# Kernel tuning notes

Hardware: AMD Instinct MI355X
Metric: run time of the kernel (lower is better)

Reference implementation:

```python
import jax, jax.numpy as jnp
import numpy as np

QMIN, QMAX = -128.0, 127.0

@jax.custom_vjp
def ste_round(x):
    return jnp.round(x)

def _ste_fwd(x):
    return jnp.round(x), None

def _ste_bwd(_, g):
    return (g,)

ste_round.defvjp(_ste_fwd, _ste_bwd)

def fake_quant_act(x, scale):
    # Int8 per-tensor fake quant: q = clip(round(x/s)) * s
    return jnp.clip(ste_round(x / scale), QMIN, QMAX) * scale

def fake_quant_weight(w):
    # Int8WeightPerTensorFloat: scale from max-abs statistic
    s = jnp.max(jnp.abs(w)) / QMAX
    return jnp.clip(ste_round(w / s), QMIN, QMAX) * s

def conv2d(x, w, b, pad):
    y = jax.lax.conv_general_dilated(
        x, w, window_strides=(1, 1), padding=[(pad, pad), (pad, pad)],
        dimension_numbers=('NCHW', 'OIHW', 'NCHW'))
    return y + b[None, :, None, None]

def maxpool2(x):
    return jax.lax.reduce_window(
        x, -jnp.inf, jax.lax.max, (1, 1, 2, 2), (1, 1, 2, 2), 'VALID')

def setup_inputs() -> dict:
    key = jax.random.key(0)
    ks = jax.random.split(key, 12)
    def w_init(k, shape, fan_in):
        return jax.random.normal(k, shape, jnp.float32) * (1.0 / np.sqrt(fan_in))
    inp = {
        'x': jax.random.normal(ks[0], (32, 1, 256, 256), jnp.float32),
        'w1': w_init(ks[1], (16, 1, 3, 3), 1 * 9),
        'b1': jax.random.normal(ks[2], (16,), jnp.float32) * 0.01,
        'w2': w_init(ks[3], (32, 16, 3, 3), 16 * 9),
        'b2': jax.random.normal(ks[4], (32,), jnp.float32) * 0.01,
        'w3': w_init(ks[5], (32, 32, 5, 5), 32 * 25),
        'b3': jax.random.normal(ks[6], (32,), jnp.float32) * 0.01,
        'w4': w_init(ks[7], (16, 32, 3, 3), 32 * 9),
        'b4': jax.random.normal(ks[8], (16,), jnp.float32) * 0.01,
        'wc': w_init(ks[9], (10, 16), 16),
        'bc': jax.random.normal(ks[10], (10,), jnp.float32) * 0.01,
        # 11 learned per-tensor activation scales, kept strictly positive
        'act_scales': jax.random.uniform(ks[11], (11,), jnp.float32) * 0.05 + 0.01,
    }
    return inp

def reference(x, w1, b1, w2, b2, w3, b3, w4, b4, wc, bc, act_scales):
    s = act_scales
    x = fake_quant_act(x, s[0])                                  # input_quant
    x = conv2d(x, fake_quant_weight(w1), b1, 0)                  # conv1 (3x3, p0)
    x = fake_quant_act(jax.nn.relu(x), s[1])                     # relu1
    x = fake_quant_act(x, s[2])                                  # quant1
    x = conv2d(x, fake_quant_weight(w2), b2, 1)                  # conv2 (3x3, p1)
    x = fake_quant_act(jax.nn.relu(x), s[3])                     # relu2
    x = fake_quant_act(x, s[4])                                  # quant2
    x = conv2d(x, fake_quant_weight(w3), b3, 2)                  # conv3 (5x5, p2)
    x = fake_quant_act(jax.nn.relu(x), s[5])                     # relu3
    x = fake_quant_act(x, s[6])                                  # quant3
    x = maxpool2(x)                                              # pool1
    x = fake_quant_act(x, s[7])                                  # pool1_quant
    x = conv2d(x, fake_quant_weight(w4), b4, 0)                  # conv4 (3x3, p0)
    x = fake_quant_act(jax.nn.relu(x), s[8])                     # relu4
    x = fake_quant_act(x, s[9])                                  # quant4
    x = jnp.mean(x, axis=(2, 3))                                 # global avg pool -> [B,16]
    x = fake_quant_act(x, s[10])                                 # pool_quant
    return x @ fake_quant_weight(wc).T + bc                      # classifier -> [B,10]
```

## Files before the change

kernel.cpp:

```cpp
#include <hip/hip_runtime.h>
#include <math.h>


typedef int i32x4  __attribute__((ext_vector_type(4)));
typedef int i32x16 __attribute__((ext_vector_type(16)));

__device__ __forceinline__ int quant_clip(float v) {
  float r = rintf(v);
  r = fminf(fmaxf(r, -128.0f), 127.0f);
  return (int)r;
}

__device__ __forceinline__ int pack4i8(int q0, int q1, int q2, int q3) {
  return (q0 & 255) | ((q1 & 255) << 8) | ((q2 & 255) << 16) | ((q3 & 255) << 24);
}

__global__ __launch_bounds__(256) void k_quant_weights(
    const float* __restrict__ w1, const float* __restrict__ w2,
    const float* __restrict__ w3, const float* __restrict__ w4,
    const float* __restrict__ wc, float* __restrict__ wscale,
    int* __restrict__ qw1, int* __restrict__ qw2B, int* __restrict__ qw3B,
    int* __restrict__ qw4B, int* __restrict__ qwc)
{
  __shared__ float red[256];
  __shared__ float ssh;
  const int t = blockIdx.x, tid = threadIdx.x;
  const float* src = (t == 0) ? w1 : (t == 1) ? w2 : (t == 2) ? w3 : (t == 3) ? w4 : wc;
  const int nsrc   = (t == 0) ? 144 : (t == 1) ? 4608 : (t == 2) ? 25600 : (t == 3) ? 4608 : 160;

  float m = 0.0f;
  for (int i = tid; i < nsrc; i += 256) m = fmaxf(m, fabsf(src[i]));
  red[tid] = m;
  __syncthreads();
  for (int s = 128; s > 0; s >>= 1) {
    if (tid < s) red[tid] = fmaxf(red[tid], red[tid + s]);
    __syncthreads();
  }
  if (tid == 0) { ssh = red[0] / 127.0f; wscale[t] = ssh; }
  __syncthreads();
  const float s = ssh;

  if (t == 0) {
    for (int i = tid; i < 144; i += 256) qw1[i] = quant_clip(w1[i] / s);
  } else if (t == 1) {
    for (int wi = tid; wi < 1536; wi += 256) {
      int step = wi >> 8, rem = wi & 255;
      int ln = rem >> 2, w = rem & 3;
      int oc = ln & 31, h = ln >> 5;
      int ky = step >> 1, kxp = (step & 1) * 2;
      int q[4];
      #pragma unroll
      for (int j = 0; j < 4; j++) {
        int k = h * 16 + w * 4 + j;
        int ic = k & 15, kx = kxp + (k >> 4);
        float val = (kx < 3) ? w2[((oc * 16 + ic) * 3 + ky) * 3 + kx] : 0.0f;
        q[j] = quant_clip(val / s);
      }
      qw2B[wi] = pack4i8(q[0], q[1], q[2], q[3]);
    }
  } else if (t == 2) {
    for (int wi = tid; wi < 6400; wi += 256) {
      int tap = wi >> 8, rem = wi & 255;
      int ln = rem >> 2, w = rem & 3;
      int oc = ln & 31, h = ln >> 5;
      int ky = tap / 5, kx = tap % 5;
      int q[4];
      #pragma unroll
      for (int j = 0; j < 4; j++) {
        int ic = h * 16 + w * 4 + j;
        q[j] = quant_clip(w3[((oc * 32 + ic) * 5 + ky) * 5 + kx] / s);
      }
      qw3B[wi] = pack4i8(q[0], q[1], q[2], q[3]);
    }
  } else if (t == 3) {
    for (int wi = tid; wi < 1280; wi += 256) {
      int mf = wi >> 8, rem = wi & 255;
      int ln = rem >> 2, w = rem & 3;
      int oc = ln & 15, chunk = ln >> 4;
      int tp = 2 * mf + (chunk >> 1);
      int half = chunk & 1;
      int q[4];
      #pragma unroll
      for (int j = 0; j < 4; j++) {
        float val = 0.0f;
        if (tp < 9) {
          int ky = tp / 3, kx = tp % 3;
          int ic = half * 16 + w * 4 + j;
          val = w4[((oc * 32 + ic) * 3 + ky) * 3 + kx];
        }
        q[j] = quant_clip(val / s);
      }
      qw4B[wi] = pack4i8(q[0], q[1], q[2], q[3]);
    }
  } else {
    for (int wi = tid; wi < 40; wi += 256) {
      int o = wi / 4, i4 = wi % 4;
      int q[4];
      #pragma unroll
      for (int j = 0; j < 4; j++) q[j] = quant_clip(wc[o * 16 + i4 * 4 + j] / s);
      qwc[wi] = pack4i8(q[0], q[1], q[2], q[3]);
    }
  }
}

__global__ __launch_bounds__(256) void k_quant_input(
    const float* __restrict__ x, const float* __restrict__ scales,
    int* __restrict__ q0w)
{
  int i = blockIdx.x * 256 + threadIdx.x;
  if (i >= 524288) return;
  float inv = 1.0f / scales[0];
  float4 v = ((const float4*)x)[i];
  q0w[i] = pack4i8(quant_clip(v.x * inv), quant_clip(v.y * inv),
                   quant_clip(v.z * inv), quant_clip(v.w * inv));
}

__global__ __launch_bounds__(256) void k_zero_border(int* __restrict__ a2p)
{
  int i = blockIdx.x * 256 + threadIdx.x;
  int n = i >> 11, p = i & 2047;
  int row, col;
  if (p < 1032) {
    int rb = p / 258;
    row = (rb < 2) ? rb : 254 + rb;
    col = p % 258;
  } else {
    int q = p - 1032;
    int cb = q & 3;
    col = (cb < 2) ? cb : 254 + cb;
    row = 2 + (q >> 2);
  }
  int4* dst = (int4*)(a2p + (((size_t)n * 258 + row) * 258 + col) * 8);
  dst[0] = make_int4(0, 0, 0, 0);
  dst[1] = make_int4(0, 0, 0, 0);
}

__global__ __launch_bounds__(256) void k_conv1(
    const signed char* __restrict__ q0, const int* __restrict__ qw1,
    const float* __restrict__ b1, const float* __restrict__ scales,
    const float* __restrict__ wscale, int* __restrict__ a1)
{
  __shared__ int wsh[144];
  __shared__ signed char lut[128];
  if (threadIdx.x < 144) wsh[threadIdx.x] = qw1[threadIdx.x];
  if (threadIdx.x < 128) {
    float s1 = scales[1], inv2 = 1.0f / scales[2];
    lut[threadIdx.x] =
        (signed char)(int)fminf(rintf(((float)threadIdx.x * s1) * inv2), 127.0f);
  }
  __syncthreads();

  int pix = blockIdx.x * 256 + threadIdx.x;
  const int TOT = 32 * 254 * 254;
  if (pix >= TOT) return;
  int n = pix / (254 * 254), r = pix % (254 * 254);
  int oy = r / 254, ox = r % 254;

  int av[9];
  const signed char* base = q0 + (n * 256 + oy) * 256 + ox;
  #pragma unroll
  for (int ky = 0; ky < 3; ky++)
    #pragma unroll
    for (int kx = 0; kx < 3; kx++)
      av[ky * 3 + kx] = (int)base[ky * 256 + kx];

  float inv1 = 1.0f / scales[1];
  float scl = scales[0] * wscale[0];
  int outw[4];
  #pragma unroll
  for (int g = 0; g < 4; g++) {
    int q[4];
    #pragma unroll
    for (int j = 0; j < 4; j++) {
      int oc = g * 4 + j;
      int acc = 0;
      #pragma unroll
      for (int k = 0; k < 9; k++) acc += av[k] * wsh[oc * 9 + k];
      float y = fmaf(scl, (float)acc, b1[oc]);
      int idx = (int)fminf(fmaxf(rintf(y * inv1), 0.0f), 127.0f);
      q[j] = lut[idx];
    }
    outw[g] = pack4i8(q[0], q[1], q[2], q[3]);
  }
  *(int4*)(a1 + pix * 4) = make_int4(outw[0], outw[1], outw[2], outw[3]);
}

__global__ __launch_bounds__(256) void k_conv2_mfma(
    const int* __restrict__ a1, const int* __restrict__ qw2B,
    const float* __restrict__ b2, const float* __restrict__ scales,
    const float* __restrict__ wscale, signed char* __restrict__ a2p)
{
  __shared__ signed char lut[128];
  if (threadIdx.x < 128) {
    float s3 = scales[3], inv4 = 1.0f / scales[4];
    lut[threadIdx.x] =
        (signed char)(int)fminf(rintf(((float)threadIdx.x * s3) * inv4), 127.0f);
  }
  __syncthreads();

  const int lane = threadIdx.x & 63;
  const int bid = blockIdx.x;
  const int swz = (bid & 7) * 256 + (bid >> 3);
  const int gw = swz * 4 + (threadIdx.x >> 6);

  i32x4 bw[6];
  #pragma unroll
  for (int t = 0; t < 6; t++)
    bw[t] = *(const i32x4*)(qw2B + (t * 64 + lane) * 4);

  const float inv3 = 1.0f / scales[3];
  const float scl = scales[2] * wscale[1];
  const int oc = lane & 31, h = lane >> 5, rr = lane & 31;
  const float bias = b2[oc];

  const int TILES = 32 * 254 * 8;
  #pragma unroll 1
  for (int t8 = 0; t8 < 8; t8++) {
    int tile = gw * 8 + t8;
    if (tile >= TILES) break;
    int n = tile / (254 * 8);
    int r = tile % (254 * 8);
    int y = r >> 3, X0 = (r & 7) * 32;

    i32x4 Af[6];
    #pragma unroll
    for (int ky = 0; ky < 3; ky++) {
      int iy = y + ky - 1;
      bool vy = (iy >= 0) && (iy < 254);
      int iyc = min(max(iy, 0), 253);
      #pragma unroll
      for (int kp = 0; kp < 2; kp++) {
        int ix = X0 + rr + kp * 2 + h - 1;
        bool vx = (ix >= 0) && (ix < 254);
        int ixc = min(max(ix, 0), 253);
        i32x4 a = *(const i32x4*)(a1 + ((n * 254 + iyc) * 254 + ixc) * 4);
        bool v = vy && vx;
        i32x4 z;
        z[0] = v ? a[0] : 0; z[1] = v ? a[1] : 0;
        z[2] = v ? a[2] : 0; z[3] = v ? a[3] : 0;
        Af[ky * 2 + kp] = z;
      }
    }

    i32x16 acc0, acc1;
    #pragma unroll
    for (int z = 0; z < 16; z++) { acc0[z] = 0; acc1[z] = 0; }
    #pragma unroll
    for (int ky = 0; ky < 3; ky++) {
      acc0 = __builtin_amdgcn_mfma_i32_32x32x32_i8(Af[ky * 2 + 0], bw[ky * 2 + 0], acc0, 0, 0, 0);
      acc1 = __builtin_amdgcn_mfma_i32_32x32x32_i8(Af[ky * 2 + 1], bw[ky * 2 + 1], acc1, 0, 0, 0);
    }

    #pragma unroll
    for (int q = 0; q < 4; q++) {
      #pragma unroll
      for (int j = 0; j < 4; j++) {
        int row = j + 8 * q + 4 * h;
        int x = X0 + row;
        int accv = acc0[q * 4 + j] + acc1[q * 4 + j];
        float yv = fmaf(scl, (float)accv, bias);
        int idx = (int)fminf(fmaxf(rintf(yv * inv3), 0.0f), 127.0f);
        if (x < 254)
          a2p[((size_t)(n * 258 + (y + 2)) * 258 + (x + 2)) * 32 + oc] =
              lut[idx];
      }
    }
  }
}

__global__ __launch_bounds__(256, 3) void k_conv3pool_mfma(
    const signed char* __restrict__ a2p, const int* __restrict__ qw3B,
    const float* __restrict__ b3, const float* __restrict__ scales,
    const float* __restrict__ wscale, signed char* __restrict__ a3p)
{
  __shared__ __align__(16) signed char ash[8 * 2176];
  __shared__ int bsh[6400];
  __shared__ signed char lut56[128];
  __shared__ signed char lut67[128];

  const int tid = threadIdx.x;
  const int lane = tid & 63;
  const int w = tid >> 6;

  const int bid = blockIdx.x;
  const int swz = (bid & 7) * 256 + (bid >> 3);
  const int n  = swz >> 6;
  const int Xg = (swz >> 4) & 3;
  const int Yq = swz & 15;
  const int c0 = 64 * Xg;

  const int oc = lane & 31, h = lane >> 5;
  const int rr = lane & 31;
  const int pp = rr >> 2, dy = (rr >> 1) & 1, dx = rr & 1;
  const int xl = 8 * w + pp;
  const int colb = (2 * xl + dx) * 32 + h * 16;
  const int X0w = 32 * Xg + 8 * w;

  const float inv5 = 1.0f / scales[5];
  const float scl = scales[4] * wscale[2];
  const float bias = b3[oc];

  {
    const int4* srcB = (const int4*)qw3B;
    int4* dstB = (int4*)bsh;
    for (int i = tid; i < 1600; i += 256) dstB[i] = srcB[i];
    if (tid < 128) {
      float s5 = scales[5], s6 = scales[6];
      float inv6 = 1.0f / s6, inv7 = 1.0f / scales[7];
      lut56[tid] = (signed char)(int)fminf(rintf(((float)tid * s5) * inv6), 127.0f);
      lut67[tid] = (signed char)(int)fminf(rintf(((float)tid * s6) * inv7), 127.0f);
    }
  }

  #pragma unroll 1
  for (int it = 0; it < 4; ++it) {
    const int Yp = 4 * Yq + it;
    const int r0 = 4 * Yp;

    __syncthreads();
    for (int ci = tid; ci < 1088; ci += 256) {
      int row = ci / 136;
      int cr = ci - row * 136;
      int col = cr >> 1, half = cr & 1;
      int gr = min(r0 + row, 257);
      int gc = min(c0 + col, 257);
      const int4* srcA = (const int4*)(a2p +
          (((size_t)n * 258 + gr) * 258 + gc) * 32 + half * 16);
      *(int4*)(&ash[row * 2176 + cr * 16]) = *srcA;
    }
    __syncthreads();

    i32x16 acc0, acc1;
    #pragma unroll
    for (int z = 0; z < 16; z++) { acc0[z] = 0; acc1[z] = 0; }

    i32x4 F0[5], F1[5], F2[5], F3[5];

#define LOAD_ROW(F, J)                                                   \
    {                                                                    \
      const signed char* rbase = &ash[(dy + (J)) * 2176 + colb];         \
      _Pragma("unroll")                                                  \
      for (int kx = 0; kx < 5; kx++)                                     \
        F[kx] = *(const i32x4*)(rbase + kx * 32);                        \
    }
#define STEP(KY, RA, RB)                                                 \
    {                                                                    \
      _Pragma("unroll")                                                  \
      for (int kx = 0; kx < 5; kx++) {                                   \
        i32x4 bfrag = *(const i32x4*)&bsh[(((KY) * 5 + kx) * 64 + lane) * 4]; \
        acc0 = __builtin_amdgcn_mfma_i32_32x32x32_i8(RA[kx], bfrag, acc0, 0, 0, 0); \
        acc1 = __builtin_amdgcn_mfma_i32_32x32x32_i8(RB[kx], bfrag, acc1, 0, 0, 0); \
      }                                                                  \
    }

    LOAD_ROW(F0, 0) LOAD_ROW(F1, 1) LOAD_ROW(F2, 2)
    LOAD_ROW(F3, 3) STEP(0, F0, F2)
    LOAD_ROW(F0, 4) STEP(1, F1, F3)
    LOAD_ROW(F1, 5) STEP(2, F2, F0)
    LOAD_ROW(F2, 6) STEP(3, F3, F1)
    STEP(4, F0, F2)
#undef LOAD_ROW
#undef STEP

    #pragma unroll
    for (int ty = 0; ty < 2; ty++) {
      int Y = 2 * Yp + ty;
      #pragma unroll
      for (int q = 0; q < 4; q++) {
        int b = 2 * q + h;
        int X = X0w + b;
        int a0, a1v, a2, a3;
        if (ty == 0) {
          a0 = acc0[q * 4 + 0]; a1v = acc0[q * 4 + 1];
          a2 = acc0[q * 4 + 2]; a3 = acc0[q * 4 + 3];
        } else {
          a0 = acc1[q * 4 + 0]; a1v = acc1[q * 4 + 1];
          a2 = acc1[q * 4 + 2]; a3 = acc1[q * 4 + 3];
        }
        int am = max(max(a0, a1v), max(a2, a3));
        float yv = fmaf(scl, (float)am, bias);
        int r1 = (int)fminf(fmaxf(rintf(yv * inv5), 0.0f), 127.0f);
        int r2 = lut56[r1];
        int r3 = lut67[r2];
        if (X < 127 && Y < 127)
          a3p[((size_t)(n * 127 + Y) * 127 + X) * 32 + oc] = (signed char)r3;
      }
    }
  }
}

__global__ __launch_bounds__(256) void k_conv4_mfma(
    const signed char* __restrict__ a3p, const int* __restrict__ qw4B,
    const float* __restrict__ b4, const float* __restrict__ scales,
    const float* __restrict__ wscale, signed char* __restrict__ a4b)
{
  __shared__ signed char lut[128];
  if (threadIdx.x < 128) {
    float s8 = scales[8], inv9 = 1.0f / scales[9];
    lut[threadIdx.x] =
        (signed char)(int)fminf(rintf(((float)threadIdx.x * s8) * inv9), 127.0f);
  }
  __syncthreads();

  const int lane = threadIdx.x & 63;
  const int bid = blockIdx.x;
  const int swz = (bid & 7) * 256 + (bid >> 3);
  const int gw = swz * 4 + (threadIdx.x >> 6);

  i32x4 bw[5];
  #pragma unroll
  for (int t = 0; t < 5; t++)
    bw[t] = *(const i32x4*)(qw4B + (t * 64 + lane) * 4);

  const int chunk = lane >> 4;
  int offB[5];
  #pragma unroll
  for (int mf = 0; mf < 5; mf++) {
    int tp = 2 * mf + (chunk >> 1);
    if (tp > 8) tp = 8;
    int ky = tp / 3, kx = tp % 3;
    offB[mf] = (ky * 127 + kx) * 32 + (chunk & 1) * 16;
  }

  const float inv8 = 1.0f / scales[8];
  const float scl = scales[7] * wscale[3];
  const int oc = lane & 15;
  const float bias = b4[oc];
  const int arow = lane & 15;

  const int TILES = 32 * 125 * 8;
  #pragma unroll 1
  for (int t4 = 0; t4 < 4; t4++) {
    int tile = gw * 4 + t4;
    if (tile >= TILES) break;
    int n = tile / 1000;
    int r = tile % 1000;
    int y = r >> 3, X0 = (r & 7) * 16;

    const signed char* base =
        a3p + ((size_t)n * 16129 + (size_t)y * 127 + (X0 + arow)) * 32;

    i32x4 Af[5];
    #pragma unroll
    for (int mf = 0; mf < 5; mf++)
      Af[mf] = *(const i32x4*)(base + offB[mf]);

    i32x4 acc;
    acc[0] = 0; acc[1] = 0; acc[2] = 0; acc[3] = 0;
    #pragma unroll
    for (int mf = 0; mf < 5; mf++)
      acc = __builtin_amdgcn_mfma_i32_16x16x64_i8(Af[mf], bw[mf], acc, 0, 0, 0);

    #pragma unroll
    for (int j = 0; j < 4; j++) {
      int x = X0 + chunk * 4 + j;
      float yv = fmaf(scl, (float)acc[j], bias);
      int idx = (int)fminf(fmaxf(rintf(yv * inv8), 0.0f), 127.0f);
      if (x < 125)
        a4b[((size_t)(n * 125 + y) * 125 + x) * 16 + oc] = lut[idx];
    }
  }
}

__global__ __launch_bounds__(256) void k_gap_stage(
    const int* __restrict__ a4, int* __restrict__ gap_acc)
{
  int img = blockIdx.x >> 4, chunk = blockIdx.x & 15;
  int tid = threadIdx.x, lane = tid & 63;
  int p0 = chunk * 977, p1 = min(p0 + 977, 15625);

  int loc[16];
  #pragma unroll
  for (int i = 0; i < 16; i++) loc[i] = 0;
  for (int p = p0 + tid; p < p1; p += 256) {
    int4 v = *(const int4*)(a4 + (img * 15625 + p) * 4);
    int w[4] = {v.x, v.y, v.z, v.w};
    #pragma unroll
    for (int wi = 0; wi < 4; wi++)
      #pragma unroll
      for (int j = 0; j < 4; j++)
        loc[wi * 4 + j] += (int)(signed char)(w[wi] >> (8 * j));
  }
  #pragma unroll
  for (int c = 0; c < 16; c++) {
    #pragma unroll
    for (int off = 32; off > 0; off >>= 1)
      loc[c] += __shfl_down(loc[c], off);
  }
  if (lane == 0) {
    #pragma unroll
    for (int c = 0; c < 16; c++) atomicAdd(&gap_acc[img * 16 + c], loc[c]);
  }
}

__global__ __launch_bounds__(64) void k_fc(
    const int* __restrict__ gap_acc, const int* __restrict__ qwc,
    const float* __restrict__ bc, const float* __restrict__ scales,
    const float* __restrict__ wscale, float* __restrict__ out)
{
  __shared__ int sq[16];
  int n = blockIdx.x, tid = threadIdx.x;
  if (tid < 16) {
    int s = gap_acc[n * 16 + tid];
    float v = scales[9] * (float)s / 15625.0f;
    float r = fminf(fmaxf(rintf(v / scales[10]), -128.0f), 127.0f);
    sq[tid] = (int)r;
  }
  __syncthreads();
  if (tid < 10) {
    int acc = 0;
    #pragma unroll
    for (int k4 = 0; k4 < 4; k4++) {
      int wv = qwc[tid * 4 + k4];
      #pragma unroll
      for (int j = 0; j < 4; j++)
        acc += sq[k4 * 4 + j] * (int)(signed char)(wv >> (8 * j));
    }
    out[n * 10 + tid] = fmaf(scales[10] * wscale[4], (float)acc, bc[tid]);
  }
}

extern "C" void kernel_launch(void* const* d_in, const int* in_sizes, int n_in,
                              void* d_out, int out_size, void* d_ws, size_t ws_size,
                              hipStream_t stream) {
  const float* x  = (const float*)d_in[0];
  const float* w1 = (const float*)d_in[1];
  const float* b1 = (const float*)d_in[2];
  const float* w2 = (const float*)d_in[3];
  const float* b2 = (const float*)d_in[4];
  const float* w3 = (const float*)d_in[5];
  const float* b3 = (const float*)d_in[6];
  const float* w4 = (const float*)d_in[7];
  const float* b4 = (const float*)d_in[8];
  const float* wc = (const float*)d_in[9];
  const float* bc = (const float*)d_in[10];
  const float* sc = (const float*)d_in[11];

  char* ws = (char*)d_ws;
  float* wscale = (float*)(ws + 0);
  int* qw1  = (int*)(ws + 64);
  int* qw2B = (int*)(ws + 1024);
  int* qw3B = (int*)(ws + 8192);
  int* qw4B = (int*)(ws + 36864);
  int* qwc  = (int*)(ws + 43008);
  int* gap_acc = (int*)(ws + 49152);
  signed char* a2p = (signed char*)(ws + 65536);
  int*  q0  = (int*)(ws + 65536);
  int*  a4  = (int*)(ws + 65536);
  int*  a1  = (int*)(ws + 68227072);
  signed char* a3p = (signed char*)(ws + 68227072);
  float* out = (float*)d_out;

  hipMemsetAsync(gap_acc, 0, 2048, stream);
  k_quant_weights<<<5, 256, 0, stream>>>(w1, w2, w3, w4, wc, wscale,
                                         qw1, qw2B, qw3B, qw4B, qwc);
  k_quant_input<<<2048, 256, 0, stream>>>(x, sc, q0);
  k_conv1<<<8065, 256, 0, stream>>>((const signed char*)q0, qw1, b1, sc, wscale, a1);
  k_zero_border<<<256, 256, 0, stream>>>((int*)a2p);
  k_conv2_mfma<<<2048, 256, 0, stream>>>(a1, qw2B, b2, sc, wscale, a2p);
  k_conv3pool_mfma<<<2048, 256, 0, stream>>>(a2p, qw3B, b3, sc, wscale, a3p);
  k_conv4_mfma<<<2048, 256, 0, stream>>>(a3p, qw4B, b4, sc, wscale,
                                         (signed char*)a4);
  k_gap_stage<<<512, 256, 0, stream>>>(a4, gap_acc);
  k_fc<<<32, 64, 0, stream>>>(gap_acc, qwc, bc, sc, wscale, out);
}
```

Measured before the change: 279.1 us.

## Stage conv2 input tile with halo in LDS for reuse across waves

Conv2 now assigns each block an 8x64 output tile, loading a 10x68 halo region of the conv1 activations into shared memory once. The four waves then read their 3x3 neighbourhoods from LDS instead of issuing repeated bounds-checked global loads for every tile. The grid doubles to 4096 blocks with fewer tiles per wave. The goal is to cut redundant global and L2 traffic from overlapping receptive fields, at the cost of an LDS fill, a barrier, and padding rows past 254 that are masked on store.

```diff
diff --git a/kernel.cpp b/kernel.cpp
--- a/kernel.cpp
+++ b/kernel.cpp
@@ -185,23 +185,37 @@
   *(int4*)(a1 + pix * 4) = make_int4(outw[0], outw[1], outw[2], outw[3]);
 }
 
-__global__ __launch_bounds__(256) void k_conv2_mfma(
+__global__ __launch_bounds__(256) void k_conv2_lds(
     const int* __restrict__ a1, const int* __restrict__ qw2B,
     const float* __restrict__ b2, const float* __restrict__ scales,
     const float* __restrict__ wscale, signed char* __restrict__ a2p)
 {
+  __shared__ __align__(16) int ash2[10 * 68 * 4];
   __shared__ signed char lut[128];
-  if (threadIdx.x < 128) {
+
+  const int tid = threadIdx.x;
+  if (tid < 128) {
     float s3 = scales[3], inv4 = 1.0f / scales[4];
-    lut[threadIdx.x] =
-        (signed char)(int)fminf(rintf(((float)threadIdx.x * s3) * inv4), 127.0f);
-  }
-  __syncthreads();
-
-  const int lane = threadIdx.x & 63;
+    lut[tid] = (signed char)(int)fminf(rintf(((float)tid * s3) * inv4), 127.0f);
+  }
+
+  const int lane = tid & 63;
+  const int w = tid >> 6;
   const int bid = blockIdx.x;
-  const int swz = (bid & 7) * 256 + (bid >> 3);
-  const int gw = swz * 4 + (threadIdx.x >> 6);
+  const int swz = (bid & 7) * 512 + (bid >> 3);
+  const int n   = swz >> 7;
+  const int rem = swz & 127;
+  const int rg = rem >> 2, cg = rem & 3;
+  const int r0 = rg * 8, c0 = cg * 64;
+
+  for (int ci = tid; ci < 680; ci += 256) {
+    int row = ci / 68, col = ci - row * 68;
+    int gr = r0 - 1 + row, gc = c0 - 1 + col;
+    i32x4 v; v[0] = 0; v[1] = 0; v[2] = 0; v[3] = 0;
+    if ((unsigned)gr < 254u && (unsigned)gc < 254u)
+      v = *(const i32x4*)(a1 + ((n * 254 + gr) * 254 + gc) * 4);
+    *(i32x4*)&ash2[ci * 4] = v;
+  }
 
   i32x4 bw[6];
   #pragma unroll
@@ -213,32 +227,21 @@
   const int oc = lane & 31, h = lane >> 5, rr = lane & 31;
   const float bias = b2[oc];
 
-  const int TILES = 32 * 254 * 8;
+  __syncthreads();
+
   #pragma unroll 1
-  for (int t8 = 0; t8 < 8; t8++) {
-    int tile = gw * 8 + t8;
-    if (tile >= TILES) break;
-    int n = tile / (254 * 8);
-    int r = tile % (254 * 8);
-    int y = r >> 3, X0 = (r & 7) * 32;
+  for (int k = 0; k < 4; k++) {
+    int s = k * 4 + w;
+    int yl = s & 7, half = s >> 3;
 
     i32x4 Af[6];
     #pragma unroll
     for (int ky = 0; ky < 3; ky++) {
-      int iy = y + ky - 1;
-      bool vy = (iy >= 0) && (iy < 254);
-      int iyc = min(max(iy, 0), 253);
       #pragma unroll
       for (int kp = 0; kp < 2; kp++) {
-        int ix = X0 + rr + kp * 2 + h - 1;
-        bool vx = (ix >= 0) && (ix < 254);
-        int ixc = min(max(ix, 0), 253);
-        i32x4 a = *(const i32x4*)(a1 + ((n * 254 + iyc) * 254 + ixc) * 4);
-        bool v = vy && vx;
-        i32x4 z;
-        z[0] = v ? a[0] : 0; z[1] = v ? a[1] : 0;
-        z[2] = v ? a[2] : 0; z[3] = v ? a[3] : 0;
-        Af[ky * 2 + kp] = z;
+        int srow = yl + ky;
+        int scol = half * 32 + rr + kp * 2 + h;
+        Af[ky * 2 + kp] = *(const i32x4*)&ash2[(srow * 68 + scol) * 4];
       }
     }
 
@@ -251,16 +254,17 @@
       acc1 = __builtin_amdgcn_mfma_i32_32x32x32_i8(Af[ky * 2 + 1], bw[ky * 2 + 1], acc1, 0, 0, 0);
     }
 
+    int y = r0 + yl;
     #pragma unroll
     for (int q = 0; q < 4; q++) {
       #pragma unroll
       for (int j = 0; j < 4; j++) {
-        int row = j + 8 * q + 4 * h;
-        int x = X0 + row;
+        int rowp = j + 8 * q + 4 * h;
+        int x = c0 + half * 32 + rowp;
         int accv = acc0[q * 4 + j] + acc1[q * 4 + j];
         float yv = fmaf(scl, (float)accv, bias);
         int idx = (int)fminf(fmaxf(rintf(yv * inv3), 0.0f), 127.0f);
-        if (x < 254)
+        if (x < 254 && y < 254)
           a2p[((size_t)(n * 258 + (y + 2)) * 258 + (x + 2)) * 32 + oc] =
               lut[idx];
       }
@@ -557,7 +561,7 @@
   k_quant_input<<<2048, 256, 0, stream>>>(x, sc, q0);
   k_conv1<<<8065, 256, 0, stream>>>((const signed char*)q0, qw1, b1, sc, wscale, a1);
   k_zero_border<<<256, 256, 0, stream>>>((int*)a2p);
-  k_conv2_mfma<<<2048, 256, 0, stream>>>(a1, qw2B, b2, sc, wscale, a2p);
+  k_conv2_lds<<<4096, 256, 0, stream>>>(a1, qw2B, b2, sc, wscale, a2p);
   k_conv3pool_mfma<<<2048, 256, 0, stream>>>(a2p, qw3B, b3, sc, wscale, a3p);
   k_conv4_mfma<<<2048, 256, 0, stream>>>(a3p, qw4B, b4, sc, wscale,
                                          (signed char*)a4);
```

After: 276.1 us. Within noise of the previous version (-1.1%).
